# Optimization experiments

Hardware: AMD Instinct MI355X
Metric: run time of the kernel (lower is better)

The kernel has to match this reference:

```python
import jax, jax.numpy as jnp
import numpy as np

B, C, H, W = 16, 256, 64, 64
LDCE, CDCE = 100, 128


def _conv(x, w, groups=1):
    # x: NCHW, w: OIHW, stride 1, SAME padding (matches pad=1 for 3x3, pad=0 for 1x1)
    return jax.lax.conv_general_dilated(x, w, (1, 1), 'SAME',
                                        feature_group_count=groups,
                                        dimension_numbers=('NCHW', 'OIHW', 'NCHW'))


def _bn(x, g, b, eps=1e-5):
    # training-mode BatchNorm2d: biased batch stats over (N,H,W)
    m = jnp.mean(x, axis=(0, 2, 3), keepdims=True)
    v = jnp.var(x, axis=(0, 2, 3), keepdims=True)
    return g[None, :, None, None] * (x - m) * jax.lax.rsqrt(v + eps) + b[None, :, None, None]


def _silu(z):
    return z * jax.nn.sigmoid(z)


def setup_inputs() -> dict:
    key = jax.random.key(0)
    ks = jax.random.split(key, 18)
    f32 = jnp.float32
    s = 0.05
    d = {}
    d['x'] = jax.random.normal(ks[0], (B, C, H, W), f32)
    d['dce_output'] = jax.random.normal(ks[1], (B, LDCE, CDCE), f32)
    # DCE projection Linear(dce_dim -> out_feat)
    d['w_dce'] = jax.random.normal(ks[2], (C, CDCE), f32) * s
    d['b_dce'] = jax.random.normal(ks[3], (C,), f32) * s
    # per-channel 3x3 convs, stacked as a depthwise kernel (C,1,3,3)
    d['w_ch'] = jax.random.normal(ks[4], (C, 1, 3, 3), f32) * s
    # shrink / expand MLP
    d['w_shrink'] = jax.random.normal(ks[5], (C // 2, C), f32) * s
    d['b_shrink'] = jax.random.normal(ks[6], (C // 2,), f32) * s
    d['w_expand'] = jax.random.normal(ks[7], (C, C // 2), f32) * s
    d['b_expand'] = jax.random.normal(ks[8], (C,), f32) * s
    # ResBlock backbone: conv3x3 -> BN -> SiLU -> conv1x1 -> BN
    d['w_conv1'] = jax.random.normal(ks[9], (C, C, 3, 3), f32) * s
    d['g_bn1'] = jnp.ones((C,), f32)
    d['be_bn1'] = jnp.zeros((C,), f32)
    d['w_conv2'] = jax.random.normal(ks[10], (C, C, 1, 1), f32) * s
    d['g_bn2'] = jnp.ones((C,), f32)
    d['be_bn2'] = jnp.zeros((C,), f32)
    # shortcut: conv1x1 -> BN
    d['w_sc'] = jax.random.normal(ks[11], (C, C, 1, 1), f32) * s
    d['g_bns'] = jnp.ones((C,), f32)
    d['be_bns'] = jnp.zeros((C,), f32)
    return d


def reference(x, dce_output, w_dce, b_dce, w_ch, w_shrink, b_shrink,
              w_expand, b_expand, w_conv1, g_bn1, be_bn1, w_conv2, g_bn2,
              be_bn2, w_sc, g_bns, be_bns):
    C2 = w_dce.shape[0]
    # 1. AdaptiveAvgPool1d(1) over sequence, then Linear: (B, C2)
    dce_pooled = jnp.mean(dce_output, axis=1)            # (B, CDCE)
    dce_proj = dce_pooled @ w_dce.T + b_dce              # (B, C2)
    # 2. per-channel Conv2d(1,1,3) + global avg pool == depthwise conv + mean
    conv_out = _conv(x, w_ch, groups=C2)                 # (B, C2, H, W)
    spatial_proj = jnp.mean(conv_out, axis=(2, 3))       # (B, C2)
    # 3-5. modulation gate
    m = dce_proj * spatial_proj
    h = jax.nn.relu(m @ w_shrink.T + b_shrink)
    mod = jax.nn.sigmoid(h @ w_expand.T + b_expand)      # (B, C2)
    # 6. channel-wise modulation
    xm = x * mod[:, :, None, None]
    # 7. ResBlock
    bb = _silu(_bn(_conv(xm, w_conv1), g_bn1, be_bn1))
    bb = _bn(_conv(bb, w_conv2), g_bn2, be_bn2)
    sc = _bn(_conv(xm, w_sc), g_bns, be_bns)
    return _silu(bb + sc)
```

## Files before the change

kernel.cpp:

```cpp
#include <hip/hip_runtime.h>

typedef unsigned short u16;
typedef unsigned int   u32;
typedef __attribute__((ext_vector_type(8))) __bf16 bf16x8;
typedef __attribute__((ext_vector_type(4))) float  f32x4;

#define HW 4096
#define NPOS 65536
#define CH 256
#define MT 512

__device__ __forceinline__ u16 f2bf(float f){
  u32 u = __float_as_uint(f);
  u += 0x7FFFu + ((u >> 16) & 1u);
  return (u16)(u >> 16);
}
__device__ __forceinline__ float bflo(u32 p){ return __uint_as_float(p << 16); }
__device__ __forceinline__ float bfhi(u32 p){ return __uint_as_float(p & 0xFFFF0000u); }

#define GLL16(g, l) __builtin_amdgcn_global_load_lds( \
    (__attribute__((address_space(1))) void*)(g), \
    (__attribute__((address_space(3))) void*)(l), 16, 0, 0)

__global__ __launch_bounds__(256) void k_statsx(const float* __restrict__ x, float* __restrict__ stats){
  int bc = blockIdx.x; int tid = threadIdx.x;
  const float* xp = x + (size_t)bc * HW;
  float S=0.f, r0=0.f, r1=0.f, c0=0.f, c1=0.f;
  #pragma unroll
  for (int k=0;k<4;k++){
    int i4 = tid + k*256;
    float4 v = ((const float4*)xp)[i4];
    int pos = i4*4; int h = pos>>6; int wb = pos&63;
    float sv = v.x+v.y+v.z+v.w;
    S += sv;
    if (h==0)  r0 += sv;
    if (h==63) r1 += sv;
    if (wb==0)  c0 += v.x;
    if (wb==60) c1 += v.w;
  }
  __shared__ float red[4][5];
  #pragma unroll
  for (int off=32; off>0; off>>=1){
    S  += __shfl_down(S, off);
    r0 += __shfl_down(r0, off);
    r1 += __shfl_down(r1, off);
    c0 += __shfl_down(c0, off);
    c1 += __shfl_down(c1, off);
  }
  if ((tid & 63) == 0){
    int w = tid >> 6;
    red[w][0]=S; red[w][1]=r0; red[w][2]=r1; red[w][3]=c0; red[w][4]=c1;
  }
  __syncthreads();
  if (tid == 0){
    float* o = stats + (size_t)bc * 9;
    for (int j=0;j<5;j++) o[j] = red[0][j]+red[1][j]+red[2][j]+red[3][j];
    o[5] = xp[0];
    o[6] = xp[63];
    o[7] = xp[4032];
    o[8] = xp[4095];
  }
}

__global__ __launch_bounds__(256) void k_gate(const float* __restrict__ dce,
    const float* __restrict__ stats, const float* __restrict__ wch,
    const float* __restrict__ w_dce, const float* __restrict__ b_dce,
    const float* __restrict__ w_sh, const float* __restrict__ b_sh,
    const float* __restrict__ w_ex, const float* __restrict__ b_ex,
    float* __restrict__ modb){
  int b = blockIdx.x, tid = threadIdx.x;
  __shared__ float pl[128];
  __shared__ float mbuf[256];
  __shared__ float hbuf[128];
  __shared__ float ptmp[256];
  {
    int k = tid & 127, half = tid >> 7;
    const float* p = dce + (size_t)b*12800 + half*50*128 + k;
    float s = 0.f;
    #pragma unroll 5
    for (int l=0;l<50;l++) s += p[l*128];
    ptmp[tid] = s;
  }
  __syncthreads();
  if (tid < 128) pl[tid] = (ptmp[tid] + ptmp[tid+128]) * 0.01f;
  __syncthreads();
  {
    int c = tid;
    const float* st = stats + (size_t)(b*256+c)*9;
    float S=st[0], r0=st[1], r1=st[2], cc0=st[3], cc1=st[4];
    float x00=st[5], x0W=st[6], xH0=st[7], xHW=st[8];
    float acc = 0.f;
    #pragma unroll
    for (int t=0;t<9;t++){
      int dh = t/3 - 1, dw = t%3 - 1;
      float R = (dh==1)? r0 : (dh==-1)? r1 : 0.f;
      float Cc = (dw==1)? cc0 : (dw==-1)? cc1 : 0.f;
      float X = 0.f;
      if (dh==1 && dw==1) X = x00;
      else if (dh==1 && dw==-1) X = x0W;
      else if (dh==-1 && dw==1) X = xH0;
      else if (dh==-1 && dw==-1) X = xHW;
      acc += wch[c*9+t] * (S - R - Cc + X);
    }
    float sp_ = acc * (1.f/4096.f);
    float dp = b_dce[c];
    const float4* wr = (const float4*)(w_dce + c*128);
    #pragma unroll 8
    for (int k4=0;k4<32;k4++){
      float4 w4 = wr[k4];
      dp += w4.x*pl[k4*4] + w4.y*pl[k4*4+1] + w4.z*pl[k4*4+2] + w4.w*pl[k4*4+3];
    }
    mbuf[c] = sp_ * dp;
  }
  __syncthreads();
  if (tid < 128){
    int j = tid;
    float acc = b_sh[j];
    const float4* wr = (const float4*)(w_sh + j*256);
    #pragma unroll 8
    for (int k4=0;k4<64;k4++){
      float4 w4 = wr[k4];
      acc += w4.x*mbuf[k4*4] + w4.y*mbuf[k4*4+1] + w4.z*mbuf[k4*4+2] + w4.w*mbuf[k4*4+3];
    }
    hbuf[j] = fmaxf(acc, 0.f);
  }
  __syncthreads();
  {
    int c = tid;
    float acc = b_ex[c];
    const float4* wr = (const float4*)(w_ex + c*128);
    #pragma unroll 8
    for (int k4=0;k4<32;k4++){
      float4 w4 = wr[k4];
      acc += w4.x*hbuf[k4*4] + w4.y*hbuf[k4*4+1] + w4.z*hbuf[k4*4+2] + w4.w*hbuf[k4*4+3];
    }
    modb[b*256+c] = 1.f/(1.f + __expf(-acc));
  }
}

__global__ __launch_bounds__(256) void k_wprep(const float* __restrict__ w1,
    const float* __restrict__ wsc, const float* __restrict__ w2,
    u16* __restrict__ w1t, u16* __restrict__ wsct, u16* __restrict__ w2t){
  int bx = blockIdx.x, ci = threadIdx.x;
  if (bx < 2304){
    int co = bx / 9, t = bx - co*9;
    w1t[(size_t)co*2304 + t*256 + ci] = f2bf(w1[(size_t)(co*256+ci)*9 + t]);
  } else if (bx < 2560){
    int i = (bx-2304)*256 + ci;
    wsct[i] = f2bf(wsc[i]);
  } else {
    int i = (bx-2560)*256 + ci;
    w2t[i] = f2bf(w2[i]);
  }
}

__global__ __launch_bounds__(256) void k_xm(const float* __restrict__ x, const float* __restrict__ modb,
                                            u16* __restrict__ xm){
  __shared__ __attribute__((aligned(16))) u16 tile[64*266];
  int pt = blockIdx.x, ct = blockIdx.y, tid = threadIdx.x;
  size_t P0 = (size_t)pt * 256;
  int b = pt >> 4;
  int rem = (pt & 15) << 8;
  int C0 = ct << 6;
  {
    int c = tid >> 2, q = tid & 3;
    const float* xp = x + ((size_t)(b*256 + C0 + c))*HW + rem;
    float mv = modb[b*256 + C0 + c];
    #pragma unroll
    for (int k=0;k<16;k++){
      int pos = q*64 + k*4;
      float4 v = *(const float4*)(xp + pos);
      u32 w0 = (u32)f2bf(v.x*mv) | ((u32)f2bf(v.y*mv) << 16);
      u32 w1 = (u32)f2bf(v.z*mv) | ((u32)f2bf(v.w*mv) << 16);
      u32* dst = (u32*)&tile[c*266 + pos];
      dst[0] = w0; dst[1] = w1;
    }
  }
  __syncthreads();
  {
    int g = tid & 7, p0 = tid >> 3;
    #pragma unroll
    for (int k=0;k<8;k++){
      int pos = p0 + k*32;
      u32 v0 = tile[(g*8+0)*266 + pos], v1 = tile[(g*8+1)*266 + pos];
      u32 v2 = tile[(g*8+2)*266 + pos], v3 = tile[(g*8+3)*266 + pos];
      u32 v4 = tile[(g*8+4)*266 + pos], v5 = tile[(g*8+5)*266 + pos];
      u32 v6 = tile[(g*8+6)*266 + pos], v7 = tile[(g*8+7)*266 + pos];
      uint4 pk;
      pk.x = v0 | (v1<<16); pk.y = v2 | (v3<<16);
      pk.z = v4 | (v5<<16); pk.w = v6 | (v7<<16);
      *(uint4*)(xm + (P0+pos)*CH + C0 + g*8) = pk;
    }
  }
}

__device__ __forceinline__ void epilogue_store(f32x4 (&acc)[4][4], int P0, int N0, int wm, int wn,
    int l15, int quad, int tid, int mt_blk, u16* __restrict__ y,
    float* __restrict__ psum, float* __restrict__ psq, float* redbuf){
  #pragma unroll
  for (int i=0;i<4;i++){
    int m = wm*64 + i*16 + quad*4;
    #pragma unroll
    for (int j=0;j<4;j++){
      int n = wn*64 + j*16 + l15;
      size_t base = ((size_t)(P0 + m))*CH + N0 + n;
      #pragma unroll
      for (int r=0;r<4;r++)
        y[base + (size_t)r*CH] = f2bf(acc[i][j][r]);
    }
  }
  #pragma unroll
  for (int j=0;j<4;j++){
    float a=0.f, b=0.f;
    #pragma unroll
    for (int i=0;i<4;i++)
      #pragma unroll
      for (int r=0;r<4;r++){ float v = acc[i][j][r]; a += v; b += v*v; }
    a += __shfl_xor(a,16); b += __shfl_xor(b,16);
    a += __shfl_xor(a,32); b += __shfl_xor(b,32);
    if (quad==0){
      int idx = (((wn*2+wm)*4 + j)*16 + l15)*2;
      redbuf[idx] = a; redbuf[idx+1] = b;
    }
  }
  __syncthreads();
  if (tid < 128){
    int n = tid; int wnn = n>>6, ntj=(n>>4)&3, li=n&15;
    int i0 = (((wnn*2+0)*4 + ntj)*16 + li)*2;
    int i1 = (((wnn*2+1)*4 + ntj)*16 + li)*2;
    psum[(size_t)(N0 + n)*MT + mt_blk] = redbuf[i0]   + redbuf[i1];
    psq [(size_t)(N0 + n)*MT + mt_blk] = redbuf[i0+1] + redbuf[i1+1];
  }
}

__global__ __launch_bounds__(256) void k_conv3(const u16* __restrict__ xm, const u16* __restrict__ w1t,
    u16* __restrict__ y, float* __restrict__ psum, float* __restrict__ psq, const u16* __restrict__ zp){
  __shared__ __attribute__((aligned(16))) u16 As[2*4096];
  __shared__ __attribute__((aligned(16))) u16 Bs[2*4096];
  __shared__ __attribute__((aligned(16))) float redbuf[512];
  int bx = blockIdx.x;
  int mt_blk = ((bx >> 4) << 3) | (bx & 7);
  int nt_blk = (bx >> 3) & 1;
  int tid = threadIdx.x;
  int lane = tid & 63, wave = tid >> 6;
  int wm = wave & 1, wn = wave >> 1;
  int l15 = lane & 15, quad = lane >> 4;
  int P0 = mt_blk*128, N0 = nt_blk*128;
  int prow = tid >> 2, cg = tid & 3;
  int cgs = cg ^ (prow & 3) ^ ((prow >> 2) & 3);
  int rdsw = (quad ^ (l15 & 3) ^ ((l15 >> 2) & 3)) * 8;
  int rA[4], rB[4];
  #pragma unroll
  for (int i=0;i<4;i++){
    rA[i] = (wm*64 + i*16 + l15)*32 + rdsw;
    rB[i] = (wn*64 + i*16 + l15)*32 + rdsw;
  }
  const u16* b0base = w1t + (size_t)(N0 + prow)*2304 + cgs*8;
  const u16* b1base = w1t + (size_t)(N0 + prow + 64)*2304 + cgs*8;
  int P_0 = P0 + prow, P_1 = P0 + prow + 64;
  int h_0 = (P_0 >> 6) & 63, w_0 = P_0 & 63, bi0 = P_0 >> 12;
  int h_1 = (P_1 >> 6) & 63, w_1 = P_1 & 63, bi1 = P_1 >> 12;

  u16* lA0 = As + wave*512;
  u16* lA1 = As + 2048 + wave*512;
  u16* lB0 = Bs + wave*512;
  u16* lB1 = Bs + 2048 + wave*512;

  f32x4 acc[4][4];
  f32x4 zz = {0.f,0.f,0.f,0.f};
  #pragma unroll
  for (int i=0;i<4;i++)
    #pragma unroll
    for (int j=0;j<4;j++) acc[i][j] = zz;

  auto aptr0 = [&](int t)->const u16*{
    int dh = t/3 - 1, dw = t%3 - 1;
    int h2 = h_0 + dh, w2 = w_0 + dw;
    return (((unsigned)h2 < 64u) && ((unsigned)w2 < 64u))
        ? xm + (((size_t)bi0*HW + h2*64 + w2)*CH) + cgs*8 : zp + cgs*8;
  };
  auto aptr1 = [&](int t)->const u16*{
    int dh = t/3 - 1, dw = t%3 - 1;
    int h2 = h_1 + dh, w2 = w_1 + dw;
    return (((unsigned)h2 < 64u) && ((unsigned)w2 < 64u))
        ? xm + (((size_t)bi1*HW + h2*64 + w2)*CH) + cgs*8 : zp + cgs*8;
  };
  auto stage = [&](const u16* a0, const u16* a1, const u16* b0, const u16* b1, int bo){
    GLL16(a0, lA0 + bo);
    GLL16(a1, lA1 + bo);
    GLL16(b0, lB0 + bo);
    GLL16(b1, lB1 + bo);
  };

  const u16 *pa0 = aptr0(0), *pa1 = aptr1(0);
  const u16 *pb0 = b0base,   *pb1 = b1base;
  stage(pa0, pa1, pb0, pb1, 0);
  __syncthreads();

  for (int t=0; t<9; t++){
    #pragma unroll
    for (int ci=0; ci<8; ci++){
      const int bo = (ci & 1) * 4096;
      if (ci < 7){
        int off = (ci+1)*32;
        stage(pa0+off, pa1+off, pb0+off, pb1+off, bo ^ 4096);
      } else if (t < 8){
        pa0 = aptr0(t+1); pa1 = aptr1(t+1);
        pb0 = b0base + (t+1)*256; pb1 = b1base + (t+1)*256;
        stage(pa0, pa1, pb0, pb1, bo ^ 4096);
      }
      bf16x8 af[4], bv[4];
      #pragma unroll
      for (int i=0;i<4;i++) af[i] = *(const bf16x8*)&As[bo + rA[i]];
      #pragma unroll
      for (int i=0;i<4;i++) bv[i] = *(const bf16x8*)&Bs[bo + rB[i]];
      #pragma unroll
      for (int i=0;i<4;i++)
        #pragma unroll
        for (int j=0;j<4;j++)
          acc[i][j] = __builtin_amdgcn_mfma_f32_16x16x32_bf16(af[i], bv[j], acc[i][j], 0, 0, 0);
      __syncthreads();
    }
  }
  epilogue_store(acc, P0, N0, wm, wn, l15, quad, tid, mt_blk, y, psum, psq, redbuf);
}

__global__ __launch_bounds__(256) void k_gemm1x1(const u16* __restrict__ A, const u16* __restrict__ Bw,
    u16* __restrict__ y, float* __restrict__ psum, float* __restrict__ psq){
  __shared__ __attribute__((aligned(16))) u16 As[2*4096];
  __shared__ __attribute__((aligned(16))) u16 Bs[2*4096];
  __shared__ __attribute__((aligned(16))) float redbuf[512];
  int bx = blockIdx.x;
  int mt_blk = ((bx >> 4) << 3) | (bx & 7);
  int nt_blk = (bx >> 3) & 1;
  int tid = threadIdx.x;
  int lane = tid & 63, wave = tid >> 6;
  int wm = wave & 1, wn = wave >> 1;
  int l15 = lane & 15, quad = lane >> 4;
  int P0 = mt_blk*128, N0 = nt_blk*128;
  int prow = tid >> 2, cg = tid & 3;
  int cgs = cg ^ (prow & 3) ^ ((prow >> 2) & 3);
  int rdsw = (quad ^ (l15 & 3) ^ ((l15 >> 2) & 3)) * 8;
  int rA[4], rB[4];
  #pragma unroll
  for (int i=0;i<4;i++){
    rA[i] = (wm*64 + i*16 + l15)*32 + rdsw;
    rB[i] = (wn*64 + i*16 + l15)*32 + rdsw;
  }
  const u16* a0p = A  + ((size_t)(P0 + prow))*CH + cgs*8;
  const u16* a1p = A  + ((size_t)(P0 + prow + 64))*CH + cgs*8;
  const u16* b0p = Bw + ((size_t)(N0 + prow))*CH + cgs*8;
  const u16* b1p = Bw + ((size_t)(N0 + prow + 64))*CH + cgs*8;

  u16* lA0 = As + wave*512;
  u16* lA1 = As + 2048 + wave*512;
  u16* lB0 = Bs + wave*512;
  u16* lB1 = Bs + 2048 + wave*512;

  f32x4 acc[4][4];
  f32x4 zz = {0.f,0.f,0.f,0.f};
  #pragma unroll
  for (int i=0;i<4;i++)
    #pragma unroll
    for (int j=0;j<4;j++) acc[i][j] = zz;

  auto stage = [&](int off, int bo){
    GLL16(a0p + off, lA0 + bo);
    GLL16(a1p + off, lA1 + bo);
    GLL16(b0p + off, lB0 + bo);
    GLL16(b1p + off, lB1 + bo);
  };

  stage(0, 0);
  __syncthreads();

  #pragma unroll
  for (int ci=0; ci<8; ci++){
    const int bo = (ci & 1) * 4096;
    if (ci < 7) stage((ci+1)*32, bo ^ 4096);
    bf16x8 af[4], bv[4];
    #pragma unroll
    for (int i=0;i<4;i++) af[i] = *(const bf16x8*)&As[bo + rA[i]];
    #pragma unroll
    for (int i=0;i<4;i++) bv[i] = *(const bf16x8*)&Bs[bo + rB[i]];
    #pragma unroll
    for (int i=0;i<4;i++)
      #pragma unroll
      for (int j=0;j<4;j++)
        acc[i][j] = __builtin_amdgcn_mfma_f32_16x16x32_bf16(af[i], bv[j], acc[i][j], 0, 0, 0);
    __syncthreads();
  }
  epilogue_store(acc, P0, N0, wm, wn, l15, quad, tid, mt_blk, y, psum, psq, redbuf);
}

__global__ __launch_bounds__(64) void k_bnstat(const float* __restrict__ psum, const float* __restrict__ psq,
    const float* __restrict__ g, const float* __restrict__ be,
    float* __restrict__ scale, float* __restrict__ shift){
  int c = blockIdx.x, t = threadIdx.x;
  const float* ps = psum + (size_t)c*MT;
  const float* pq = psq  + (size_t)c*MT;
  float s=0.f, q=0.f;
  #pragma unroll
  for (int i=0;i<8;i++){ s += ps[t + i*64]; q += pq[t + i*64]; }
  #pragma unroll
  for (int off=32; off>0; off>>=1){
    s += __shfl_down(s, off);
    q += __shfl_down(q, off);
  }
  if (t == 0){
    float mean = s * (1.f/65536.f);
    float var  = q * (1.f/65536.f) - mean*mean;
    float rstd = rsqrtf(var + 1e-5f);
    float sc = g[c]*rstd;
    scale[c] = sc;
    shift[c] = be[c] - mean*sc;
  }
}

__global__ __launch_bounds__(256) void k_bb(const u16* __restrict__ y1, const float* __restrict__ sc1,
    const float* __restrict__ sh1, u16* __restrict__ bb){
  __shared__ float sc[256], sh[256];
  int tid = threadIdx.x;
  sc[tid] = sc1[tid]; sh[tid] = sh1[tid];
  __syncthreads();
  size_t i = ((size_t)blockIdx.x*256 + tid)*8;
  int c0 = (int)(i & 255);
  uint4 v = *(const uint4*)(y1 + i);
  u32 a[4] = {v.x, v.y, v.z, v.w};
  u32 o[4];
  #pragma unroll
  for (int p=0;p<4;p++){
    float zl = sc[c0+2*p]*bflo(a[p]) + sh[c0+2*p];
    float zh = sc[c0+2*p+1]*bfhi(a[p]) + sh[c0+2*p+1];
    float ol = zl/(1.f+__expf(-zl));
    float oh = zh/(1.f+__expf(-zh));
    o[p] = (u32)f2bf(ol) | ((u32)f2bf(oh) << 16);
  }
  uint4 w; w.x=o[0]; w.y=o[1]; w.z=o[2]; w.w=o[3];
  *(uint4*)(bb + i) = w;
}

__global__ __launch_bounds__(256) void k_final(const u16* __restrict__ y2, const u16* __restrict__ ysc,
    const float* __restrict__ sc2, const float* __restrict__ sh2,
    const float* __restrict__ scs, const float* __restrict__ shs,
    float* __restrict__ out){
  __shared__ __attribute__((aligned(16))) float tile[64*257];
  __shared__ float l2s[64], l2h[64], lss[64], lsh[64];
  int pt = blockIdx.x, ct = blockIdx.y, tid = threadIdx.x;
  int C0 = ct << 6;
  if (tid < 64){ l2s[tid]=sc2[C0+tid]; l2h[tid]=sh2[C0+tid]; lss[tid]=scs[C0+tid]; lsh[tid]=shs[C0+tid]; }
  __syncthreads();
  size_t P0 = (size_t)pt * 256;
  int b = pt >> 4; int rem = (pt & 15) << 8;
  {
    int g = tid & 7, p0 = tid >> 3;
    for (int k=0;k<8;k++){
      int pos = p0 + k*32;
      size_t off = (P0+pos)*CH + C0 + g*8;
      uint4 va = *(const uint4*)(y2 + off);
      uint4 vb = *(const uint4*)(ysc + off);
      u32 aa[4] = {va.x,va.y,va.z,va.w};
      u32 bv[4] = {vb.x,vb.y,vb.z,vb.w};
      #pragma unroll
      for (int p=0;p<4;p++){
        int c = g*8 + 2*p;
        float z0 = l2s[c]*bflo(aa[p]) + l2h[c] + lss[c]*bflo(bv[p]) + lsh[c];
        float z1 = l2s[c+1]*bfhi(aa[p]) + l2h[c+1] + lss[c+1]*bfhi(bv[p]) + lsh[c+1];
        tile[c*257 + pos]     = z0/(1.f+__expf(-z0));
        tile[(c+1)*257 + pos] = z1/(1.f+__expf(-z1));
      }
    }
  }
  __syncthreads();
  {
    int c = tid >> 2, q = tid & 3;
    float* op = out + ((size_t)(b*256 + C0 + c))*HW + rem;
    #pragma unroll
    for (int k=0;k<16;k++){
      int pos = q*64 + k*4;
      float4 v;
      v.x = tile[c*257 + pos];
      v.y = tile[c*257 + pos + 1];
      v.z = tile[c*257 + pos + 2];
      v.w = tile[c*257 + pos + 3];
      *(float4*)(op + pos) = v;
    }
  }
}

extern "C" void kernel_launch(void* const* d_in, const int* in_sizes, int n_in,
                              void* d_out, int out_size, void* d_ws, size_t ws_size,
                              hipStream_t stream){
  const float* x     = (const float*)d_in[0];
  const float* dce   = (const float*)d_in[1];
  const float* w_dce = (const float*)d_in[2];
  const float* b_dce = (const float*)d_in[3];
  const float* w_ch  = (const float*)d_in[4];
  const float* w_sh  = (const float*)d_in[5];
  const float* b_sh  = (const float*)d_in[6];
  const float* w_ex  = (const float*)d_in[7];
  const float* b_ex  = (const float*)d_in[8];
  const float* w_c1  = (const float*)d_in[9];
  const float* g1    = (const float*)d_in[10];
  const float* be1   = (const float*)d_in[11];
  const float* w_c2  = (const float*)d_in[12];
  const float* g2    = (const float*)d_in[13];
  const float* be2   = (const float*)d_in[14];
  const float* w_s   = (const float*)d_in[15];
  const float* gs    = (const float*)d_in[16];
  const float* bes   = (const float*)d_in[17];
  float* out = (float*)d_out;
  char* ws = (char*)d_ws;

  const size_t NB = (size_t)NPOS*CH*2;
  u16* xm  = (u16*)(ws);
  u16* y1  = (u16*)(ws + NB);
  u16* ysc = (u16*)(ws + 2*NB);
  u16* bb  = (u16*)(ws + 3*NB);
  char* p = ws + 4*NB;
  u16* w1t   = (u16*)p; p += (size_t)256*2304*2;
  u16* wsct  = (u16*)p; p += (size_t)256*256*2;
  u16* w2t   = (u16*)p; p += (size_t)256*256*2;
  float* statsx = (float*)p; p += (size_t)16*256*9*4;
  float* modb   = (float*)p; p += (size_t)16*256*4;
  float* p1s = (float*)p; p += (size_t)MT*256*4;
  float* p1q = (float*)p; p += (size_t)MT*256*4;
  float* pss = (float*)p; p += (size_t)MT*256*4;
  float* psqv= (float*)p; p += (size_t)MT*256*4;
  float* p2s = (float*)p; p += (size_t)MT*256*4;
  float* p2q = (float*)p; p += (size_t)MT*256*4;
  float* bn1sc = (float*)p; p += 1024;
  float* bn1sh = (float*)p; p += 1024;
  float* bnssc = (float*)p; p += 1024;
  float* bnssh = (float*)p; p += 1024;
  float* bn2sc = (float*)p; p += 1024;
  float* bn2sh = (float*)p; p += 1024;
  u16* zp = (u16*)p; p += 4096;

  hipMemsetAsync(zp, 0, 4096, stream);
  k_statsx<<<4096, 256, 0, stream>>>(x, statsx);
  k_wprep<<<2816, 256, 0, stream>>>(w_c1, w_s, w_c2, w1t, wsct, w2t);
  k_gate<<<16, 256, 0, stream>>>(dce, statsx, w_ch, w_dce, b_dce, w_sh, b_sh, w_ex, b_ex, modb);
  k_xm<<<dim3(256,4), 256, 0, stream>>>(x, modb, xm);
  k_conv3<<<1024, 256, 0, stream>>>(xm, w1t, y1, p1s, p1q, zp);
  k_bnstat<<<256, 64, 0, stream>>>(p1s, p1q, g1, be1, bn1sc, bn1sh);
  k_bb<<<8192, 256, 0, stream>>>(y1, bn1sc, bn1sh, bb);
  k_gemm1x1<<<1024, 256, 0, stream>>>(xm, wsct, ysc, pss, psqv);
  k_bnstat<<<256, 64, 0, stream>>>(pss, psqv, gs, bes, bnssc, bnssh);
  k_gemm1x1<<<1024, 256, 0, stream>>>(bb, w2t, y1 , p2s, p2q);
  k_bnstat<<<256, 64, 0, stream>>>(p2s, p2q, g2, be2, bn2sc, bn2sh);
  k_final<<<dim3(256,4), 256, 0, stream>>>(y1, ysc, bn2sc, bn2sh, bnssc, bnssh, out);
}
```

Baseline: 431.2 us.

## Triple-buffer LDS tiles with vmcnt waits and single barrier per step

Both the 3x3 conv and the 1x1 GEMM kernels move from double to triple LDS buffering. Loads run two K-chunks ahead, and each iteration uses partial s_waitcnt vmcnt(4) instead of waiting on everything. The two __syncthreads per step become one raw barrier placed before the next stage is issued. The goal is to hide global-to-LDS load latency behind the MFMA work and cut barrier stalls, at the cost of 50% more LDS per block, which may lower occupancy.

Result: no change. 425.6 us (-1.3%).

```diff
diff --git a/kernel.cpp b/kernel.cpp
--- a/kernel.cpp
+++ b/kernel.cpp
@@ -21,6 +21,10 @@
 #define GLL16(g, l) __builtin_amdgcn_global_load_lds( \
     (__attribute__((address_space(1))) void*)(g), \
     (__attribute__((address_space(3))) void*)(l), 16, 0, 0)
+
+#define VM4() asm volatile("s_waitcnt vmcnt(4)" ::: "memory")
+#define VM0() asm volatile("s_waitcnt vmcnt(0)" ::: "memory")
+#define RBAR() do { __builtin_amdgcn_s_barrier(); __builtin_amdgcn_sched_barrier(0); } while(0)
 
 __global__ __launch_bounds__(256) void k_statsx(const float* __restrict__ x, float* __restrict__ stats){
   int bc = blockIdx.x; int tid = threadIdx.x;
@@ -235,8 +239,8 @@
 
 __global__ __launch_bounds__(256) void k_conv3(const u16* __restrict__ xm, const u16* __restrict__ w1t,
     u16* __restrict__ y, float* __restrict__ psum, float* __restrict__ psq, const u16* __restrict__ zp){
-  __shared__ __attribute__((aligned(16))) u16 As[2*4096];
-  __shared__ __attribute__((aligned(16))) u16 Bs[2*4096];
+  __shared__ __attribute__((aligned(16))) u16 As[3*4096];
+  __shared__ __attribute__((aligned(16))) u16 Bs[3*4096];
   __shared__ __attribute__((aligned(16))) float redbuf[512];
   int bx = blockIdx.x;
   int mt_blk = ((bx >> 4) << 3) | (bx & 7);
@@ -261,11 +265,6 @@
   int h_0 = (P_0 >> 6) & 63, w_0 = P_0 & 63, bi0 = P_0 >> 12;
   int h_1 = (P_1 >> 6) & 63, w_1 = P_1 & 63, bi1 = P_1 >> 12;
 
-  u16* lA0 = As + wave*512;
-  u16* lA1 = As + 2048 + wave*512;
-  u16* lB0 = Bs + wave*512;
-  u16* lB1 = Bs + 2048 + wave*512;
-
   f32x4 acc[4][4];
   f32x4 zz = {0.f,0.f,0.f,0.f};
   #pragma unroll
@@ -286,49 +285,67 @@
         ? xm + (((size_t)bi1*HW + h2*64 + w2)*CH) + cgs*8 : zp + cgs*8;
   };
   auto stage = [&](const u16* a0, const u16* a1, const u16* b0, const u16* b1, int bo){
-    GLL16(a0, lA0 + bo);
-    GLL16(a1, lA1 + bo);
-    GLL16(b0, lB0 + bo);
-    GLL16(b1, lB1 + bo);
+    GLL16(a0, As + bo + wave*512);
+    GLL16(a1, As + bo + 2048 + wave*512);
+    GLL16(b0, Bs + bo + wave*512);
+    GLL16(b1, Bs + bo + 2048 + wave*512);
   };
 
-  const u16 *pa0 = aptr0(0), *pa1 = aptr1(0);
-  const u16 *pb0 = b0base,   *pb1 = b1base;
-  stage(pa0, pa1, pb0, pb1, 0);
-  __syncthreads();
-
-  for (int t=0; t<9; t++){
-    #pragma unroll
-    for (int ci=0; ci<8; ci++){
-      const int bo = (ci & 1) * 4096;
-      if (ci < 7){
-        int off = (ci+1)*32;
-        stage(pa0+off, pa1+off, pb0+off, pb1+off, bo ^ 4096);
-      } else if (t < 8){
-        pa0 = aptr0(t+1); pa1 = aptr1(t+1);
-        pb0 = b0base + (t+1)*256; pb1 = b1base + (t+1)*256;
-        stage(pa0, pa1, pb0, pb1, bo ^ 4096);
+  const u16 *sa0 = aptr0(0), *sa1 = aptr1(0);
+  const u16 *sb0 = b0base,   *sb1 = b1base;
+  const u16 *na0 = sa0, *na1 = sa1, *nb0 = sb0, *nb1 = sb1;
+
+  stage(sa0,      sa1,      sb0,      sb1,      0);
+  stage(sa0 + 32, sa1 + 32, sb0 + 32, sb1 + 32, 4096);
+  int woff = 8192, roff = 0;
+
+  for (int t=0; t<9; ++t){
+    #pragma unroll
+    for (int ci=0; ci<8; ++ci){
+      if (ci == 7){
+        if (t == 8) { VM0(); } else { VM4(); }
+      } else {
+        VM4();
       }
+      RBAR();
+      if (t < 8 || ci < 6){
+        const u16 *pa0s, *pa1s, *pb0s, *pb1s;
+        if (ci < 6){
+          pa0s = sa0 + (ci+2)*32; pa1s = sa1 + (ci+2)*32;
+          pb0s = sb0 + (ci+2)*32; pb1s = sb1 + (ci+2)*32;
+        } else if (ci == 6){
+          na0 = aptr0(t+1); na1 = aptr1(t+1);
+          nb0 = b0base + (t+1)*256; nb1 = b1base + (t+1)*256;
+          pa0s = na0; pa1s = na1; pb0s = nb0; pb1s = nb1;
+        } else {
+          pa0s = na0 + 32; pa1s = na1 + 32;
+          pb0s = nb0 + 32; pb1s = nb1 + 32;
+        }
+        stage(pa0s, pa1s, pb0s, pb1s, woff);
+        woff = (woff == 8192) ? 0 : (woff + 4096);
+      }
+      if (ci == 7 && t < 8){ sa0 = na0; sa1 = na1; sb0 = nb0; sb1 = nb1; }
       bf16x8 af[4], bv[4];
       #pragma unroll
-      for (int i=0;i<4;i++) af[i] = *(const bf16x8*)&As[bo + rA[i]];
-      #pragma unroll
-      for (int i=0;i<4;i++) bv[i] = *(const bf16x8*)&Bs[bo + rB[i]];
+      for (int i=0;i<4;i++) af[i] = *(const bf16x8*)&As[roff + rA[i]];
+      #pragma unroll
+      for (int i=0;i<4;i++) bv[i] = *(const bf16x8*)&Bs[roff + rB[i]];
       #pragma unroll
       for (int i=0;i<4;i++)
         #pragma unroll
         for (int j=0;j<4;j++)
           acc[i][j] = __builtin_amdgcn_mfma_f32_16x16x32_bf16(af[i], bv[j], acc[i][j], 0, 0, 0);
-      __syncthreads();
-    }
-  }
+      roff = (roff == 8192) ? 0 : (roff + 4096);
+    }
+  }
+  __syncthreads();
   epilogue_store(acc, P0, N0, wm, wn, l15, quad, tid, mt_blk, y, psum, psq, redbuf);
 }
 
 __global__ __launch_bounds__(256) void k_gemm1x1(const u16* __restrict__ A, const u16* __restrict__ Bw,
     u16* __restrict__ y, float* __restrict__ psum, float* __restrict__ psq){
-  __shared__ __attribute__((aligned(16))) u16 As[2*4096];
-  __shared__ __attribute__((aligned(16))) u16 Bs[2*4096];
+  __shared__ __attribute__((aligned(16))) u16 As[3*4096];
+  __shared__ __attribute__((aligned(16))) u16 Bs[3*4096];
   __shared__ __attribute__((aligned(16))) float redbuf[512];
   int bx = blockIdx.x;
   int mt_blk = ((bx >> 4) << 3) | (bx & 7);
@@ -352,11 +369,6 @@
   const u16* b0p = Bw + ((size_t)(N0 + prow))*CH + cgs*8;
   const u16* b1p = Bw + ((size_t)(N0 + prow + 64))*CH + cgs*8;
 
-  u16* lA0 = As + wave*512;
-  u16* lA1 = As + 2048 + wave*512;
-  u16* lB0 = Bs + wave*512;
-  u16* lB1 = Bs + 2048 + wave*512;
-
   f32x4 acc[4][4];
   f32x4 zz = {0.f,0.f,0.f,0.f};
   #pragma unroll
@@ -365,31 +377,37 @@
     for (int j=0;j<4;j++) acc[i][j] = zz;
 
   auto stage = [&](int off, int bo){
-    GLL16(a0p + off, lA0 + bo);
-    GLL16(a1p + off, lA1 + bo);
-    GLL16(b0p + off, lB0 + bo);
-    GLL16(b1p + off, lB1 + bo);
+    GLL16(a0p + off, As + bo + wave*512);
+    GLL16(a1p + off, As + bo + 2048 + wave*512);
+    GLL16(b0p + off, Bs + bo + wave*512);
+    GLL16(b1p + off, Bs + bo + 2048 + wave*512);
   };
 
   stage(0, 0);
-  __syncthreads();
-
-  #pragma unroll
-  for (int ci=0; ci<8; ci++){
-    const int bo = (ci & 1) * 4096;
-    if (ci < 7) stage((ci+1)*32, bo ^ 4096);
+  stage(32, 4096);
+  int woff = 8192, roff = 0;
+
+  #pragma unroll
+  for (int ci=0; ci<8; ++ci){
+    if (ci == 7) { VM0(); } else { VM4(); }
+    RBAR();
+    if (ci < 6){
+      stage((ci+2)*32, woff);
+      woff = (woff == 8192) ? 0 : (woff + 4096);
+    }
     bf16x8 af[4], bv[4];
     #pragma unroll
-    for (int i=0;i<4;i++) af[i] = *(const bf16x8*)&As[bo + rA[i]];
-    #pragma unroll
-    for (int i=0;i<4;i++) bv[i] = *(const bf16x8*)&Bs[bo + rB[i]];
+    for (int i=0;i<4;i++) af[i] = *(const bf16x8*)&As[roff + rA[i]];
+    #pragma unroll
+    for (int i=0;i<4;i++) bv[i] = *(const bf16x8*)&Bs[roff + rB[i]];
     #pragma unroll
     for (int i=0;i<4;i++)
       #pragma unroll
       for (int j=0;j<4;j++)
         acc[i][j] = __builtin_amdgcn_mfma_f32_16x16x32_bf16(af[i], bv[j], acc[i][j], 0, 0, 0);
-    __syncthreads();
-  }
+    roff = (roff == 8192) ? 0 : (roff + 4096);
+  }
+  __syncthreads();
   epilogue_store(acc, P0, N0, wm, wn, l15, quad, tid, mt_blk, y, psum, psq, redbuf);
 }
 
```

## Replace conv/GEMM kernels with 256x256-tile 8-wave GEMM using 4-stage LDS pipeline

Applied to the files above, without the earlier changes.

Replaces the 128x128-tile, 4-wave conv3x3 and 1x1 GEMM kernels with one templated kernel. It uses 256x256 output tiles, 8 waves, and a 4-deep global_load_lds ring buffer with explicit vmcnt waits, split barriers and setprio around the MFMA groups. Larger tiles raise arithmetic intensity and cut re-reads of the A operand across N tiles. The trade-offs are 128KB of LDS per block and only 256 blocks, which may underfill the CUs or limit occupancy. The partial-stat layout shrinks from 512 to 256 M-tiles per channel, and bnstat is adjusted to match.

Result: faster. 393.3 us (-8.8%).

```diff
diff --git a/kernel.cpp b/kernel.cpp
--- a/kernel.cpp
+++ b/kernel.cpp
@@ -9,6 +9,7 @@
 #define NPOS 65536
 #define CH 256
 #define MT 512
+#define NMT 256
 
 __device__ __forceinline__ u16 f2bf(float f){
   u32 u = __float_as_uint(f);
@@ -21,6 +22,11 @@
 #define GLL16(g, l) __builtin_amdgcn_global_load_lds( \
     (__attribute__((address_space(1))) void*)(g), \
     (__attribute__((address_space(3))) void*)(l), 16, 0, 0)
+
+#define VM8() asm volatile("s_waitcnt vmcnt(8)" ::: "memory")
+#define VM4() asm volatile("s_waitcnt vmcnt(4)" ::: "memory")
+#define VM0() asm volatile("s_waitcnt vmcnt(0)" ::: "memory")
+#define BARX() do { __builtin_amdgcn_s_barrier(); __builtin_amdgcn_sched_barrier(0); } while(0)
 
 __global__ __launch_bounds__(256) void k_statsx(const float* __restrict__ x, float* __restrict__ stats){
   int bc = blockIdx.x; int tid = threadIdx.x;
@@ -194,214 +200,154 @@
   }
 }
 
-__device__ __forceinline__ void epilogue_store(f32x4 (&acc)[4][4], int P0, int N0, int wm, int wn,
-    int l15, int quad, int tid, int mt_blk, u16* __restrict__ y,
-    float* __restrict__ psum, float* __restrict__ psq, float* redbuf){
-  #pragma unroll
-  for (int i=0;i<4;i++){
-    int m = wm*64 + i*16 + quad*4;
+template<int NTAPS>
+__global__ __launch_bounds__(512, 2) void k_gemm8p(const u16* __restrict__ A,
+    const u16* __restrict__ Bw, u16* __restrict__ y,
+    float* __restrict__ psum, float* __restrict__ psq, const u16* __restrict__ zp){
+  constexpr int KTOT = NTAPS*256;
+  constexpr int NT = KTOT/32;
+  __shared__ __attribute__((aligned(16))) u16 SH[65536];
+  int tid = threadIdx.x;
+  int lane = tid & 63, wave = tid >> 6;
+  int wm = wave >> 2, wn = wave & 3;
+  int l15 = lane & 15, quad = lane >> 4;
+  int mt = blockIdx.x;
+  int P0 = mt*256;
+
+  int rdx   = (((l15>>3)&1)<<4) | (((l15>>2)&1)<<3);
+  int kphys = (quad*8) ^ rdx;
+  int aoff  = (wm*128 + l15)*32 + kphys;
+  int boff  = 32768 + (wn*64 + l15)*32 + kphys;
+
+  int pr = tid >> 2;
+  int kb = (tid&3) ^ ((((tid>>5)&1)<<1) | ((tid>>4)&1));
+  int k0 = kb*8;
+  int pos0 = P0 + pr, pos1 = P0 + 128 + pr;
+  int hh0 = (pos0>>6)&63, ww0 = pos0&63;
+  int hh1 = (pos1>>6)&63, ww1 = pos1&63;
+
+  f32x4 acc[8][4];
+  f32x4 zz = {0.f,0.f,0.f,0.f};
+  #pragma unroll
+  for (int i=0;i<8;i++)
+    #pragma unroll
+    for (int j=0;j<4;j++) acc[i][j] = zz;
+
+  auto stageA = [&](int ktn){
+    int set = ktn & 3;
+    if constexpr (NTAPS == 9){
+      int tap = ktn >> 3;
+      int t3 = tap/3;
+      int dh = t3 - 1, dw = (tap - t3*3) - 1;
+      int d = dh*64 + dw;
+      int coff = ((ktn & 7)*32) + k0;
+      bool ok0 = ((unsigned)(hh0+dh) < 64u) && ((unsigned)(ww0+dw) < 64u);
+      bool ok1 = ((unsigned)(hh1+dh) < 64u) && ((unsigned)(ww1+dw) < 64u);
+      const u16* s0 = ok0 ? A + (size_t)(pos0 + d)*CH + coff : zp + coff;
+      const u16* s1 = ok1 ? A + (size_t)(pos1 + d)*CH + coff : zp + coff;
+      GLL16(s0, SH + set*8192 + wave*512);
+      GLL16(s1, SH + set*8192 + 4096 + wave*512);
+    } else {
+      const u16* s0 = A + (size_t)pos0*CH + ktn*32 + k0;
+      const u16* s1 = A + (size_t)pos1*CH + ktn*32 + k0;
+      GLL16(s0, SH + set*8192 + wave*512);
+      GLL16(s1, SH + set*8192 + 4096 + wave*512);
+    }
+  };
+  auto stageB = [&](int ktn){
+    int set = ktn & 3;
+    const u16* s0 = Bw + (size_t)pr*KTOT + ktn*32 + k0;
+    const u16* s1 = Bw + (size_t)(pr+128)*KTOT + ktn*32 + k0;
+    GLL16(s0, SH + 32768 + set*8192 + wave*512);
+    GLL16(s1, SH + 32768 + set*8192 + 4096 + wave*512);
+  };
+
+  stageA(0); stageB(0);
+  stageA(1); stageB(1);
+  stageA(2); stageB(2);
+  VM8();
+  BARX();
+
+  for (int w = 0; w < NT; ++w){
+    int sb = (w & 3)*8192;
+    bf16x8 af[4], bv[4];
+    #pragma unroll
+    for (int i=0;i<4;i++) af[i] = *(const bf16x8*)&SH[sb + aoff + i*512];
+    #pragma unroll
+    for (int j=0;j<4;j++) bv[j] = *(const bf16x8*)&SH[sb + boff + j*512];
+    if (w+3 < NT) stageA(w+3);
+    BARX();
+    __builtin_amdgcn_s_setprio(1);
+    #pragma unroll
+    for (int i=0;i<4;i++)
+      #pragma unroll
+      for (int j=0;j<4;j++)
+        acc[i][j] = __builtin_amdgcn_mfma_f32_16x16x32_bf16(af[i], bv[j], acc[i][j], 0, 0, 0);
+    __builtin_amdgcn_s_setprio(0);
+    BARX();
+    #pragma unroll
+    for (int i=0;i<4;i++) af[i] = *(const bf16x8*)&SH[sb + aoff + 2048 + i*512];
+    if (w+3 < NT) stageB(w+3);
+    if (w < NT-3)      { VM8(); }
+    else if (w == NT-3){ VM4(); }
+    else if (w == NT-2){ VM0(); }
+    BARX();
+    __builtin_amdgcn_s_setprio(1);
+    #pragma unroll
+    for (int i=0;i<4;i++)
+      #pragma unroll
+      for (int j=0;j<4;j++)
+        acc[4+i][j] = __builtin_amdgcn_mfma_f32_16x16x32_bf16(af[i], bv[j], acc[4+i][j], 0, 0, 0);
+    __builtin_amdgcn_s_setprio(0);
+    BARX();
+  }
+
+  #pragma unroll
+  for (int i=0;i<8;i++){
+    int m = wm*128 + i*16 + quad*4;
     #pragma unroll
     for (int j=0;j<4;j++){
       int n = wn*64 + j*16 + l15;
-      size_t base = ((size_t)(P0 + m))*CH + N0 + n;
+      size_t base = ((size_t)(P0 + m))*CH + n;
       #pragma unroll
       for (int r=0;r<4;r++)
         y[base + (size_t)r*CH] = f2bf(acc[i][j][r]);
     }
   }
+  float* SHf = (float*)SH;
   #pragma unroll
   for (int j=0;j<4;j++){
     float a=0.f, b=0.f;
     #pragma unroll
-    for (int i=0;i<4;i++)
+    for (int i=0;i<8;i++)
       #pragma unroll
       for (int r=0;r<4;r++){ float v = acc[i][j][r]; a += v; b += v*v; }
     a += __shfl_xor(a,16); b += __shfl_xor(b,16);
     a += __shfl_xor(a,32); b += __shfl_xor(b,32);
     if (quad==0){
-      int idx = (((wn*2+wm)*4 + j)*16 + l15)*2;
-      redbuf[idx] = a; redbuf[idx+1] = b;
-    }
-  }
-  __syncthreads();
-  if (tid < 128){
-    int n = tid; int wnn = n>>6, ntj=(n>>4)&3, li=n&15;
-    int i0 = (((wnn*2+0)*4 + ntj)*16 + li)*2;
-    int i1 = (((wnn*2+1)*4 + ntj)*16 + li)*2;
-    psum[(size_t)(N0 + n)*MT + mt_blk] = redbuf[i0]   + redbuf[i1];
-    psq [(size_t)(N0 + n)*MT + mt_blk] = redbuf[i0+1] + redbuf[i1+1];
-  }
-}
-
-__global__ __launch_bounds__(256) void k_conv3(const u16* __restrict__ xm, const u16* __restrict__ w1t,
-    u16* __restrict__ y, float* __restrict__ psum, float* __restrict__ psq, const u16* __restrict__ zp){
-  __shared__ __attribute__((aligned(16))) u16 As[2*4096];
-  __shared__ __attribute__((aligned(16))) u16 Bs[2*4096];
-  __shared__ __attribute__((aligned(16))) float redbuf[512];
-  int bx = blockIdx.x;
-  int mt_blk = ((bx >> 4) << 3) | (bx & 7);
-  int nt_blk = (bx >> 3) & 1;
-  int tid = threadIdx.x;
-  int lane = tid & 63, wave = tid >> 6;
-  int wm = wave & 1, wn = wave >> 1;
-  int l15 = lane & 15, quad = lane >> 4;
-  int P0 = mt_blk*128, N0 = nt_blk*128;
-  int prow = tid >> 2, cg = tid & 3;
-  int cgs = cg ^ (prow & 3) ^ ((prow >> 2) & 3);
-  int rdsw = (quad ^ (l15 & 3) ^ ((l15 >> 2) & 3)) * 8;
-  int rA[4], rB[4];
-  #pragma unroll
-  for (int i=0;i<4;i++){
-    rA[i] = (wm*64 + i*16 + l15)*32 + rdsw;
-    rB[i] = (wn*64 + i*16 + l15)*32 + rdsw;
-  }
-  const u16* b0base = w1t + (size_t)(N0 + prow)*2304 + cgs*8;
-  const u16* b1base = w1t + (size_t)(N0 + prow + 64)*2304 + cgs*8;
-  int P_0 = P0 + prow, P_1 = P0 + prow + 64;
-  int h_0 = (P_0 >> 6) & 63, w_0 = P_0 & 63, bi0 = P_0 >> 12;
-  int h_1 = (P_1 >> 6) & 63, w_1 = P_1 & 63, bi1 = P_1 >> 12;
-
-  u16* lA0 = As + wave*512;
-  u16* lA1 = As + 2048 + wave*512;
-  u16* lB0 = Bs + wave*512;
-  u16* lB1 = Bs + 2048 + wave*512;
-
-  f32x4 acc[4][4];
-  f32x4 zz = {0.f,0.f,0.f,0.f};
-  #pragma unroll
-  for (int i=0;i<4;i++)
-    #pragma unroll
-    for (int j=0;j<4;j++) acc[i][j] = zz;
-
-  auto aptr0 = [&](int t)->const u16*{
-    int dh = t/3 - 1, dw = t%3 - 1;
-    int h2 = h_0 + dh, w2 = w_0 + dw;
-    return (((unsigned)h2 < 64u) && ((unsigned)w2 < 64u))
-        ? xm + (((size_t)bi0*HW + h2*64 + w2)*CH) + cgs*8 : zp + cgs*8;
-  };
-  auto aptr1 = [&](int t)->const u16*{
-    int dh = t/3 - 1, dw = t%3 - 1;
-    int h2 = h_1 + dh, w2 = w_1 + dw;
-    return (((unsigned)h2 < 64u) && ((unsigned)w2 < 64u))
-        ? xm + (((size_t)bi1*HW + h2*64 + w2)*CH) + cgs*8 : zp + cgs*8;
-  };
-  auto stage = [&](const u16* a0, const u16* a1, const u16* b0, const u16* b1, int bo){
-    GLL16(a0, lA0 + bo);
-    GLL16(a1, lA1 + bo);
-    GLL16(b0, lB0 + bo);
-    GLL16(b1, lB1 + bo);
-  };
-
-  const u16 *pa0 = aptr0(0), *pa1 = aptr1(0);
-  const u16 *pb0 = b0base,   *pb1 = b1base;
-  stage(pa0, pa1, pb0, pb1, 0);
-  __syncthreads();
-
-  for (int t=0; t<9; t++){
-    #pragma unroll
-    for (int ci=0; ci<8; ci++){
-      const int bo = (ci & 1) * 4096;
-      if (ci < 7){
-        int off = (ci+1)*32;
-        stage(pa0+off, pa1+off, pb0+off, pb1+off, bo ^ 4096);
-      } else if (t < 8){
-        pa0 = aptr0(t+1); pa1 = aptr1(t+1);
-        pb0 = b0base + (t+1)*256; pb1 = b1base + (t+1)*256;
-        stage(pa0, pa1, pb0, pb1, bo ^ 4096);
-      }
-      bf16x8 af[4], bv[4];
-      #pragma unroll
-      for (int i=0;i<4;i++) af[i] = *(const bf16x8*)&As[bo + rA[i]];
-      #pragma unroll
-      for (int i=0;i<4;i++) bv[i] = *(const bf16x8*)&Bs[bo + rB[i]];
-      #pragma unroll
-      for (int i=0;i<4;i++)
-        #pragma unroll
-        for (int j=0;j<4;j++)
-          acc[i][j] = __builtin_amdgcn_mfma_f32_16x16x32_bf16(af[i], bv[j], acc[i][j], 0, 0, 0);
-      __syncthreads();
-    }
-  }
-  epilogue_store(acc, P0, N0, wm, wn, l15, quad, tid, mt_blk, y, psum, psq, redbuf);
-}
-
-__global__ __launch_bounds__(256) void k_gemm1x1(const u16* __restrict__ A, const u16* __restrict__ Bw,
-    u16* __restrict__ y, float* __restrict__ psum, float* __restrict__ psq){
-  __shared__ __attribute__((aligned(16))) u16 As[2*4096];
-  __shared__ __attribute__((aligned(16))) u16 Bs[2*4096];
-  __shared__ __attribute__((aligned(16))) float redbuf[512];
-  int bx = blockIdx.x;
-  int mt_blk = ((bx >> 4) << 3) | (bx & 7);
-  int nt_blk = (bx >> 3) & 1;
-  int tid = threadIdx.x;
-  int lane = tid & 63, wave = tid >> 6;
-  int wm = wave & 1, wn = wave >> 1;
-  int l15 = lane & 15, quad = lane >> 4;
-  int P0 = mt_blk*128, N0 = nt_blk*128;
-  int prow = tid >> 2, cg = tid & 3;
-  int cgs = cg ^ (prow & 3) ^ ((prow >> 2) & 3);
-  int rdsw = (quad ^ (l15 & 3) ^ ((l15 >> 2) & 3)) * 8;
-  int rA[4], rB[4];
-  #pragma unroll
-  for (int i=0;i<4;i++){
-    rA[i] = (wm*64 + i*16 + l15)*32 + rdsw;
-    rB[i] = (wn*64 + i*16 + l15)*32 + rdsw;
-  }
-  const u16* a0p = A  + ((size_t)(P0 + prow))*CH + cgs*8;
-  const u16* a1p = A  + ((size_t)(P0 + prow + 64))*CH + cgs*8;
-  const u16* b0p = Bw + ((size_t)(N0 + prow))*CH + cgs*8;
-  const u16* b1p = Bw + ((size_t)(N0 + prow + 64))*CH + cgs*8;
-
-  u16* lA0 = As + wave*512;
-  u16* lA1 = As + 2048 + wave*512;
-  u16* lB0 = Bs + wave*512;
-  u16* lB1 = Bs + 2048 + wave*512;
-
-  f32x4 acc[4][4];
-  f32x4 zz = {0.f,0.f,0.f,0.f};
-  #pragma unroll
-  for (int i=0;i<4;i++)
-    #pragma unroll
-    for (int j=0;j<4;j++) acc[i][j] = zz;
-
-  auto stage = [&](int off, int bo){
-    GLL16(a0p + off, lA0 + bo);
-    GLL16(a1p + off, lA1 + bo);
-    GLL16(b0p + off, lB0 + bo);
-    GLL16(b1p + off, lB1 + bo);
-  };
-
-  stage(0, 0);
-  __syncthreads();
-
-  #pragma unroll
-  for (int ci=0; ci<8; ci++){
-    const int bo = (ci & 1) * 4096;
-    if (ci < 7) stage((ci+1)*32, bo ^ 4096);
-    bf16x8 af[4], bv[4];
-    #pragma unroll
-    for (int i=0;i<4;i++) af[i] = *(const bf16x8*)&As[bo + rA[i]];
-    #pragma unroll
-    for (int i=0;i<4;i++) bv[i] = *(const bf16x8*)&Bs[bo + rB[i]];
-    #pragma unroll
-    for (int i=0;i<4;i++)
-      #pragma unroll
-      for (int j=0;j<4;j++)
-        acc[i][j] = __builtin_amdgcn_mfma_f32_16x16x32_bf16(af[i], bv[j], acc[i][j], 0, 0, 0);
-    __syncthreads();
-  }
-  epilogue_store(acc, P0, N0, wm, wn, l15, quad, tid, mt_blk, y, psum, psq, redbuf);
+      int idx = ((wave*4 + j)*16 + l15)*2;
+      SHf[idx] = a; SHf[idx+1] = b;
+    }
+  }
+  __syncthreads();
+  if (tid < 256){
+    int n = tid; int wnn = n>>6; int j = (n>>4)&3; int li = n&15;
+    int i0 = (((wnn)*4 + j)*16 + li)*2;
+    int i1 = (((4+wnn)*4 + j)*16 + li)*2;
+    psum[(size_t)n*NMT + mt] = SHf[i0] + SHf[i1];
+    psq [(size_t)n*NMT + mt] = SHf[i0+1] + SHf[i1+1];
+  }
 }
 
 __global__ __launch_bounds__(64) void k_bnstat(const float* __restrict__ psum, const float* __restrict__ psq,
     const float* __restrict__ g, const float* __restrict__ be,
     float* __restrict__ scale, float* __restrict__ shift){
   int c = blockIdx.x, t = threadIdx.x;
-  const float* ps = psum + (size_t)c*MT;
-  const float* pq = psq  + (size_t)c*MT;
+  const float* ps = psum + (size_t)c*NMT;
+  const float* pq = psq  + (size_t)c*NMT;
   float s=0.f, q=0.f;
   #pragma unroll
-  for (int i=0;i<8;i++){ s += ps[t + i*64]; q += pq[t + i*64]; }
+  for (int i=0;i<4;i++){ s += ps[t + i*64]; q += pq[t + i*64]; }
   #pragma unroll
   for (int off=32; off>0; off>>=1){
     s += __shfl_down(s, off);
@@ -542,12 +488,12 @@
   k_wprep<<<2816, 256, 0, stream>>>(w_c1, w_s, w_c2, w1t, wsct, w2t);
   k_gate<<<16, 256, 0, stream>>>(dce, statsx, w_ch, w_dce, b_dce, w_sh, b_sh, w_ex, b_ex, modb);
   k_xm<<<dim3(256,4), 256, 0, stream>>>(x, modb, xm);
-  k_conv3<<<1024, 256, 0, stream>>>(xm, w1t, y1, p1s, p1q, zp);
+  k_gemm8p<9><<<256, 512, 0, stream>>>(xm, w1t, y1, p1s, p1q, zp);
   k_bnstat<<<256, 64, 0, stream>>>(p1s, p1q, g1, be1, bn1sc, bn1sh);
   k_bb<<<8192, 256, 0, stream>>>(y1, bn1sc, bn1sh, bb);
-  k_gemm1x1<<<1024, 256, 0, stream>>>(xm, wsct, ysc, pss, psqv);
+  k_gemm8p<1><<<256, 512, 0, stream>>>(xm, wsct, ysc, pss, psqv, zp);
   k_bnstat<<<256, 64, 0, stream>>>(pss, psqv, gs, bes, bnssc, bnssh);
-  k_gemm1x1<<<1024, 256, 0, stream>>>(bb, w2t, y1 , p2s, p2q);
+  k_gemm8p<1><<<256, 512, 0, stream>>>(bb, w2t, y1 , p2s, p2q, zp);
   k_bnstat<<<256, 64, 0, stream>>>(p2s, p2q, g2, be2, bn2sc, bn2sh);
   k_final<<<dim3(256,4), 256, 0, stream>>>(y1, ysc, bn2sc, bn2sh, bnssc, bnssh, out);
 }
```
